# Kernel optimization log

Measured on AMD Instinct MI355X. Metric: run time of the kernel, lower is better.

The kernel has to match this reference:

```python
import jax, jax.numpy as jnp
import numpy as np

B, D, P, E, C = 2048, 4096, 64, 8, 64
K = D // P  # conv kernel = stride = input_dim / patch_num


def setup_inputs() -> dict:
    key = jax.random.key(0)
    k1, k2, k3, k4 = jax.random.split(key, 4)
    x = jax.random.normal(k1, (B, 1, D), jnp.float32)
    router_w = jax.random.normal(k2, (E, K), jnp.float32) * 0.02   # Router conv weight [E,1,K] squeezed
    expert_w = jax.random.normal(k3, (E, 2 * C, K), jnp.float32) * 0.001  # per-expert conv weights (small=True scaling)
    expert_b = jax.random.normal(k4, (E, 2 * C), jnp.float32) * 0.001
    return {"x": x, "router_w": router_w, "expert_w": expert_w, "expert_b": expert_b}


def reference(x, router_w, expert_w, expert_b):
    b, _, d = x.shape
    e, k = router_w.shape
    p = d // k
    c = expert_w.shape[1] // 2

    # Conv1d(1, ch, K, stride=K) == per-patch matmul; sum over dim 2 == sum over patches.
    patches = x.reshape(b, p, k)                                   # [B,P,K]

    # Router (eval mode: no noise)
    select = jnp.einsum('bpk,ek->be', patches, router_w)           # [B,E]

    # top1 routing
    gate = jnp.max(select, axis=-1)                                # [B]
    index = jnp.argmax(select, axis=-1)                            # [B]
    onehot = jax.nn.one_hot(index, e, dtype=select.dtype)          # [B,E]

    # aux load-balance loss
    density = onehot.mean(axis=0)
    density_proxy = select.mean(axis=0)
    loss = (density_proxy * density).mean() * float(e ** 2)

    # combine/dispatch (mask_flat is all ones for top1)
    combine = gate[:, None] * onehot                               # [B,E]
    dispatch = jax.lax.stop_gradient((combine != 0).astype(select.dtype))  # bool cast detaches grad
    select0 = dispatch

    # Dense dispatch: every expert sees the full batch, zero-masked by dispatch.
    # z[e,b,c,p] = conv of (dispatch[b,e]*x[b]) with expert e's kernel, + bias
    z = jnp.einsum('bpk,eck->ebcp', patches, expert_w)             # [E,B,2C,P]
    z = z * dispatch.T[:, :, None, None] + expert_b[:, None, :, None]
    z = z ** 3                                                     # nonlinear=True
    s = z.sum(axis=-1)                                             # sum over patches -> [E,B,2C]
    expert_out = jnp.stack([s[..., :c].sum(-1), s[..., c:].sum(-1)], axis=-1)  # [E,B,2]

    out = jnp.einsum('be,ebl->bl', combine, expert_out)            # [B,2]
    out = jax.nn.softmax(out, axis=1)
    return out, select0, loss
```

## Files before the change

kernel.cpp:

```cpp
#include <hip/hip_runtime.h>

#define BB 2048
#define DD 4096
#define PP 64
#define KK 64
#define EE 8
#define C2 128

typedef __attribute__((ext_vector_type(8))) short short8;
typedef __attribute__((ext_vector_type(4))) float floatx4;

__device__ inline unsigned short f2bf(float f) {
    unsigned int u = __builtin_bit_cast(unsigned int, f);
    u += 0x7FFFu + ((u >> 16) & 1u);
    return (unsigned short)(u >> 16);
}
__device__ inline unsigned pack2_trunc(float lo, float hi) {
    unsigned ul = __builtin_bit_cast(unsigned, lo);
    unsigned uh = __builtin_bit_cast(unsigned, hi);
    return (uh & 0xFFFF0000u) | (ul >> 16);
}

__global__ __launch_bounds__(256) void prep_w(const float* __restrict__ ew,
                                              unsigned short* __restrict__ wbf) {
    int idx = blockIdx.x * 256 + threadIdx.x;
    float4 v = ((const float4*)ew)[idx];
    ushort4 o;
    o.x = f2bf(v.x); o.y = f2bf(v.y); o.z = f2bf(v.z); o.w = f2bf(v.w);
    ((ushort4*)wbf)[idx] = o;
}

__global__ __launch_bounds__(256) void moe3(
    const float* __restrict__ x, const float* __restrict__ rw,
    const unsigned short* __restrict__ wbf, const float* __restrict__ eb,
    float* __restrict__ out, float* __restrict__ ws_sel)
{
    const int lane = threadIdx.x & 63;
    const int b = blockIdx.x * 4 + (threadIdx.x >> 6);
    const int r = lane & 15, q = lane >> 4;
    const float* xb = x + (size_t)b * DD;

    float ps[16];
    #pragma unroll
    for (int j = 0; j < 16; ++j) ps[j] = 0.f;
    short8 af[8];
    #pragma unroll
    for (int mt = 0; mt < 4; ++mt) {
        #pragma unroll
        for (int kb = 0; kb < 2; ++kb) {
            const float* base = xb + (mt * 16 + r) * 64 + kb * 32 + q * 8;
            float4 v0 = *(const float4*)base;
            float4 v1 = *(const float4*)(base + 4);
            ps[kb*8+0] += v0.x; ps[kb*8+1] += v0.y; ps[kb*8+2] += v0.z; ps[kb*8+3] += v0.w;
            ps[kb*8+4] += v1.x; ps[kb*8+5] += v1.y; ps[kb*8+6] += v1.z; ps[kb*8+7] += v1.w;
            uint4 u;
            u.x = pack2_trunc(v0.x, v0.y); u.y = pack2_trunc(v0.z, v0.w);
            u.z = pack2_trunc(v1.x, v1.y); u.w = pack2_trunc(v1.z, v1.w);
            af[mt * 2 + kb] = __builtin_bit_cast(short8, u);
        }
    }

    float d[8];
    #pragma unroll
    for (int e2 = 0; e2 < 8; ++e2) {
        const float* rwe = rw + e2 * KK;
        float4 a0 = *(const float4*)(rwe + q * 8);
        float4 a1 = *(const float4*)(rwe + q * 8 + 4);
        float4 b0 = *(const float4*)(rwe + 32 + q * 8);
        float4 b1 = *(const float4*)(rwe + 32 + q * 8 + 4);
        float t = ps[0]*a0.x + ps[1]*a0.y + ps[2]*a0.z + ps[3]*a0.w
                + ps[4]*a1.x + ps[5]*a1.y + ps[6]*a1.z + ps[7]*a1.w
                + ps[8]*b0.x + ps[9]*b0.y + ps[10]*b0.z + ps[11]*b0.w
                + ps[12]*b1.x + ps[13]*b1.y + ps[14]*b1.z + ps[15]*b1.w;
        t += __shfl_xor(t, 1);  t += __shfl_xor(t, 2);  t += __shfl_xor(t, 4);
        t += __shfl_xor(t, 8);  t += __shfl_xor(t, 16); t += __shfl_xor(t, 32);
        d[e2] = t;
    }
    float gate = d[0]; int e = 0;
    #pragma unroll
    for (int e2 = 1; e2 < 8; ++e2)
        if (d[e2] > gate) { gate = d[e2]; e = e2; }

    if (lane == 0) {
        float4 s0 = make_float4(d[0], d[1], d[2], d[3]);
        float4 s1 = make_float4(d[4], d[5], d[6], d[7]);
        *(float4*)(ws_sel + b * 8)     = s0;
        *(float4*)(ws_sel + b * 8 + 4) = s1;
        float on = (gate != 0.f) ? 1.f : 0.f;
        float4 o0 = make_float4(e==0?on:0.f, e==1?on:0.f, e==2?on:0.f, e==3?on:0.f);
        float4 o1 = make_float4(e==4?on:0.f, e==5?on:0.f, e==6?on:0.f, e==7?on:0.f);
        *(float4*)(out + BB * 2 + b * 8)     = o0;
        *(float4*)(out + BB * 2 + b * 8 + 4) = o1;
    }

    const unsigned short* we = wbf + (size_t)e * (C2 * KK);
    float h0 = 0.f, h1 = 0.f;
    #pragma unroll
    for (int nt = 0; nt < 8; ++nt) {
        float bs = eb[e * C2 + nt * 16 + r];
        const unsigned short* wr = we + (nt * 16 + r) * KK + q * 8;
        short8 bf0 = *(const short8*)wr;
        short8 bf1 = *(const short8*)(wr + 32);
        #pragma unroll
        for (int mt = 0; mt < 4; ++mt) {
            floatx4 acc = (floatx4){0.f, 0.f, 0.f, 0.f};
            acc = __builtin_amdgcn_mfma_f32_16x16x32_bf16(af[mt*2+0], bf0, acc, 0, 0, 0);
            acc = __builtin_amdgcn_mfma_f32_16x16x32_bf16(af[mt*2+1], bf1, acc, 0, 0, 0);
            float hh = 0.f;
            #pragma unroll
            for (int i = 0; i < 4; ++i) {
                float z = acc[i] + bs;
                hh = fmaf(z * z, z, hh);
            }
            if (nt < 4) h0 += hh; else h1 += hh;
        }
    }
    #pragma unroll
    for (int off = 1; off < 64; off <<= 1) {
        h0 += __shfl_xor(h0, off);
        h1 += __shfl_xor(h1, off);
    }
    if (lane == 0) {
        float l0 = gate * h0, l1 = gate * h1;
        float m = fmaxf(l0, l1);
        float e0 = __expf(l0 - m), e1 = __expf(l1 - m);
        float inv = 1.f / (e0 + e1);
        float2 o; o.x = e0 * inv; o.y = e1 * inv;
        *(float2*)(out + b * 2) = o;
    }
}

__global__ __launch_bounds__(256) void loss_kernel(
    const float* __restrict__ ws_sel, float* __restrict__ out)
{
    __shared__ float red[4][16];
    const int t = threadIdx.x;
    const int w = t >> 6, lane = t & 63;

    float p[8] = {0,0,0,0,0,0,0,0};
    float c[8] = {0,0,0,0,0,0,0,0};
    #pragma unroll
    for (int it = 0; it < BB / 256; ++it) {
        int b = it * 256 + t;
        const float4* row = (const float4*)(ws_sel + b * 8);
        float4 r0 = row[0], r1 = row[1];
        float v[8] = {r0.x, r0.y, r0.z, r0.w, r1.x, r1.y, r1.z, r1.w};
        float g = v[0]; int ix = 0;
        #pragma unroll
        for (int e2 = 1; e2 < 8; ++e2)
            if (v[e2] > g) { g = v[e2]; ix = e2; }
        #pragma unroll
        for (int e2 = 0; e2 < 8; ++e2) p[e2] += v[e2];
        c[ix] += 1.f;
    }
    #pragma unroll
    for (int off = 32; off > 0; off >>= 1) {
        #pragma unroll
        for (int e2 = 0; e2 < 8; ++e2) {
            p[e2] += __shfl_xor(p[e2], off);
            c[e2] += __shfl_xor(c[e2], off);
        }
    }
    if (lane == 0) {
        #pragma unroll
        for (int e2 = 0; e2 < 8; ++e2) { red[w][e2] = p[e2]; red[w][8 + e2] = c[e2]; }
    }
    __syncthreads();
    if (t == 0) {
        float loss = 0.f;
        #pragma unroll
        for (int e2 = 0; e2 < 8; ++e2) {
            float sp = red[0][e2] + red[1][e2] + red[2][e2] + red[3][e2];
            float sc = red[0][8 + e2] + red[1][8 + e2] + red[2][8 + e2] + red[3][8 + e2];
            loss += (sp / (float)BB) * (sc / (float)BB);
        }
        out[BB * 2 + BB * 8] = loss * (float)EE;
    }
}

extern "C" void kernel_launch(void* const* d_in, const int* in_sizes, int n_in,
                              void* d_out, int out_size, void* d_ws, size_t ws_size,
                              hipStream_t stream) {
    (void)in_sizes; (void)n_in; (void)out_size; (void)ws_size;
    const float* x  = (const float*)d_in[0];
    const float* rw = (const float*)d_in[1];
    const float* ew = (const float*)d_in[2];
    const float* eb = (const float*)d_in[3];
    float* out = (float*)d_out;
    float* ws_sel = (float*)d_ws;
    unsigned short* wbf = (unsigned short*)((char*)d_ws + BB * EE * 4);

    prep_w<<<64, 256, 0, stream>>>(ew, wbf);
    moe3<<<BB / 4, 256, 0, stream>>>(x, rw, wbf, eb, out, ws_sel);
    loss_kernel<<<1, 256, 0, stream>>>(ws_sel, out);
}
```

Baseline: 92.91 us.

## Fuse weight conversion and loss reduction into a single MoE kernel

Drops the separate bf16 weight-prep kernel and instead truncates fp32 expert weights to bf16 inside the main kernel as they are loaded. The separate single-block loss kernel is replaced by per-block atomic partial sums into a small workspace, plus a last-block-done counter that finalizes the loss. This removes two kernel launches and the global round trip of the select matrix, but adds a memset, global atomics, and twice the weight bytes read per wave. Weight rounding changes from round-to-nearest to truncation.

```diff
diff --git a/kernel.cpp b/kernel.cpp
--- a/kernel.cpp
+++ b/kernel.cpp
@@ -6,37 +6,31 @@
 #define KK 64
 #define EE 8
 #define C2 128
+#define NBLK (BB / 4)
 
 typedef __attribute__((ext_vector_type(8))) short short8;
 typedef __attribute__((ext_vector_type(4))) float floatx4;
 
-__device__ inline unsigned short f2bf(float f) {
-    unsigned int u = __builtin_bit_cast(unsigned int, f);
-    u += 0x7FFFu + ((u >> 16) & 1u);
-    return (unsigned short)(u >> 16);
-}
 __device__ inline unsigned pack2_trunc(float lo, float hi) {
     unsigned ul = __builtin_bit_cast(unsigned, lo);
     unsigned uh = __builtin_bit_cast(unsigned, hi);
     return (uh & 0xFFFF0000u) | (ul >> 16);
 }
 
-__global__ __launch_bounds__(256) void prep_w(const float* __restrict__ ew,
-                                              unsigned short* __restrict__ wbf) {
-    int idx = blockIdx.x * 256 + threadIdx.x;
-    float4 v = ((const float4*)ew)[idx];
-    ushort4 o;
-    o.x = f2bf(v.x); o.y = f2bf(v.y); o.z = f2bf(v.z); o.w = f2bf(v.w);
-    ((ushort4*)wbf)[idx] = o;
-}
+__global__ __launch_bounds__(256) void moe_all(
+    const float* __restrict__ x, const float* __restrict__ rw,
+    const float* __restrict__ ew, const float* __restrict__ eb,
+    float* __restrict__ out, float* __restrict__ acc)
+{
+    __shared__ float wred[4][8];
+    __shared__ int   wred_i[4];
+    __shared__ unsigned lastv;
+    __shared__ float fin[128];
 
-__global__ __launch_bounds__(256) void moe3(
-    const float* __restrict__ x, const float* __restrict__ rw,
-    const unsigned short* __restrict__ wbf, const float* __restrict__ eb,
-    float* __restrict__ out, float* __restrict__ ws_sel)
-{
-    const int lane = threadIdx.x & 63;
-    const int b = blockIdx.x * 4 + (threadIdx.x >> 6);
+    const int tid  = threadIdx.x;
+    const int lane = tid & 63;
+    const int w    = tid >> 6;
+    const int b    = blockIdx.x * 4 + w;
     const int r = lane & 15, q = lane >> 4;
     const float* xb = x + (size_t)b * DD;
 
@@ -82,10 +76,6 @@
         if (d[e2] > gate) { gate = d[e2]; e = e2; }
 
     if (lane == 0) {
-        float4 s0 = make_float4(d[0], d[1], d[2], d[3]);
-        float4 s1 = make_float4(d[4], d[5], d[6], d[7]);
-        *(float4*)(ws_sel + b * 8)     = s0;
-        *(float4*)(ws_sel + b * 8 + 4) = s1;
         float on = (gate != 0.f) ? 1.f : 0.f;
         float4 o0 = make_float4(e==0?on:0.f, e==1?on:0.f, e==2?on:0.f, e==3?on:0.f);
         float4 o1 = make_float4(e==4?on:0.f, e==5?on:0.f, e==6?on:0.f, e==7?on:0.f);
@@ -93,23 +83,32 @@
         *(float4*)(out + BB * 2 + b * 8 + 4) = o1;
     }
 
-    const unsigned short* we = wbf + (size_t)e * (C2 * KK);
+    const float* we = ew + (size_t)e * (C2 * KK);
     float h0 = 0.f, h1 = 0.f;
     #pragma unroll
     for (int nt = 0; nt < 8; ++nt) {
         float bs = eb[e * C2 + nt * 16 + r];
-        const unsigned short* wr = we + (nt * 16 + r) * KK + q * 8;
-        short8 bf0 = *(const short8*)wr;
-        short8 bf1 = *(const short8*)(wr + 32);
+        const float* wr = we + (nt * 16 + r) * KK + q * 8;
+        float4 w0 = *(const float4*)wr;
+        float4 w1 = *(const float4*)(wr + 4);
+        float4 w2 = *(const float4*)(wr + 32);
+        float4 w3 = *(const float4*)(wr + 36);
+        uint4 u0, u1;
+        u0.x = pack2_trunc(w0.x, w0.y); u0.y = pack2_trunc(w0.z, w0.w);
+        u0.z = pack2_trunc(w1.x, w1.y); u0.w = pack2_trunc(w1.z, w1.w);
+        u1.x = pack2_trunc(w2.x, w2.y); u1.y = pack2_trunc(w2.z, w2.w);
+        u1.z = pack2_trunc(w3.x, w3.y); u1.w = pack2_trunc(w3.z, w3.w);
+        short8 bf0 = __builtin_bit_cast(short8, u0);
+        short8 bf1 = __builtin_bit_cast(short8, u1);
         #pragma unroll
         for (int mt = 0; mt < 4; ++mt) {
-            floatx4 acc = (floatx4){0.f, 0.f, 0.f, 0.f};
-            acc = __builtin_amdgcn_mfma_f32_16x16x32_bf16(af[mt*2+0], bf0, acc, 0, 0, 0);
-            acc = __builtin_amdgcn_mfma_f32_16x16x32_bf16(af[mt*2+1], bf1, acc, 0, 0, 0);
+            floatx4 a4 = (floatx4){0.f, 0.f, 0.f, 0.f};
+            a4 = __builtin_amdgcn_mfma_f32_16x16x32_bf16(af[mt*2+0], bf0, a4, 0, 0, 0);
+            a4 = __builtin_amdgcn_mfma_f32_16x16x32_bf16(af[mt*2+1], bf1, a4, 0, 0, 0);
             float hh = 0.f;
             #pragma unroll
             for (int i = 0; i < 4; ++i) {
-                float z = acc[i] + bs;
+                float z = a4[i] + bs;
                 hh = fmaf(z * z, z, hh);
             }
             if (nt < 4) h0 += hh; else h1 += hh;
@@ -128,53 +127,46 @@
         float2 o; o.x = e0 * inv; o.y = e1 * inv;
         *(float2*)(out + b * 2) = o;
     }
-}
 
-__global__ __launch_bounds__(256) void loss_kernel(
-    const float* __restrict__ ws_sel, float* __restrict__ out)
-{
-    __shared__ float red[4][16];
-    const int t = threadIdx.x;
-    const int w = t >> 6, lane = t & 63;
-
-    float p[8] = {0,0,0,0,0,0,0,0};
-    float c[8] = {0,0,0,0,0,0,0,0};
-    #pragma unroll
-    for (int it = 0; it < BB / 256; ++it) {
-        int b = it * 256 + t;
-        const float4* row = (const float4*)(ws_sel + b * 8);
-        float4 r0 = row[0], r1 = row[1];
-        float v[8] = {r0.x, r0.y, r0.z, r0.w, r1.x, r1.y, r1.z, r1.w};
-        float g = v[0]; int ix = 0;
-        #pragma unroll
-        for (int e2 = 1; e2 < 8; ++e2)
-            if (v[e2] > g) { g = v[e2]; ix = e2; }
-        #pragma unroll
-        for (int e2 = 0; e2 < 8; ++e2) p[e2] += v[e2];
-        c[ix] += 1.f;
-    }
-    #pragma unroll
-    for (int off = 32; off > 0; off >>= 1) {
-        #pragma unroll
-        for (int e2 = 0; e2 < 8; ++e2) {
-            p[e2] += __shfl_xor(p[e2], off);
-            c[e2] += __shfl_xor(c[e2], off);
-        }
-    }
     if (lane == 0) {
         #pragma unroll
-        for (int e2 = 0; e2 < 8; ++e2) { red[w][e2] = p[e2]; red[w][8 + e2] = c[e2]; }
+        for (int j = 0; j < 8; ++j) wred[w][j] = d[j];
+        wred_i[w] = e;
     }
     __syncthreads();
-    if (t == 0) {
-        float loss = 0.f;
-        #pragma unroll
-        for (int e2 = 0; e2 < 8; ++e2) {
-            float sp = red[0][e2] + red[1][e2] + red[2][e2] + red[3][e2];
-            float sc = red[0][8 + e2] + red[1][8 + e2] + red[2][8 + e2] + red[3][8 + e2];
-            loss += (sp / (float)BB) * (sc / (float)BB);
+    if (tid < 16) {
+        float v;
+        if (tid < 8) {
+            v = wred[0][tid] + wred[1][tid] + wred[2][tid] + wred[3][tid];
+        } else {
+            int ee = tid - 8;
+            v = (float)((wred_i[0]==ee) + (wred_i[1]==ee) + (wred_i[2]==ee) + (wred_i[3]==ee));
         }
-        out[BB * 2 + BB * 8] = loss * (float)EE;
+        atomicAdd(&acc[(blockIdx.x & 7) * 16 + tid], v);
+    }
+    __syncthreads();
+    if (tid == 0) {
+        __threadfence();
+        lastv = atomicAdd((unsigned*)(acc + 128), 1u);
+    }
+    __syncthreads();
+    if (lastv == (unsigned)(NBLK - 1)) {
+        if (tid < 128) fin[tid] = atomicAdd(&acc[tid], 0.f);
+        __syncthreads();
+        if (tid == 0) {
+            float loss = 0.f;
+            #pragma unroll
+            for (int e2 = 0; e2 < 8; ++e2) {
+                float sp = 0.f, sc = 0.f;
+                #pragma unroll
+                for (int bk = 0; bk < 8; ++bk) {
+                    sp += fin[bk * 16 + e2];
+                    sc += fin[bk * 16 + 8 + e2];
+                }
+                loss += (sp / (float)BB) * (sc / (float)BB);
+            }
+            out[BB * 2 + BB * 8] = loss * (float)EE;
+        }
     }
 }
 
@@ -187,10 +179,8 @@
     const float* ew = (const float*)d_in[2];
     const float* eb = (const float*)d_in[3];
     float* out = (float*)d_out;
-    float* ws_sel = (float*)d_ws;
-    unsigned short* wbf = (unsigned short*)((char*)d_ws + BB * EE * 4);
+    float* acc = (float*)d_ws;
 
-    prep_w<<<64, 256, 0, stream>>>(ew, wbf);
-    moe3<<<BB / 4, 256, 0, stream>>>(x, rw, wbf, eb, out, ws_sel);
-    loss_kernel<<<1, 256, 0, stream>>>(ws_sel, out);
+    hipMemsetAsync(acc, 0, 129 * sizeof(float), stream);
+    moe_all<<<NBLK, 256, 0, stream>>>(x, rw, ew, eb, out, acc);
 }
```

New measurement: 103.2 us. +11.1%, slower.
